# Kernel tuning notes

Hardware: AMD Instinct MI355X
Metric: run time of the kernel (lower is better)

## Reference

```python
import jax, jax.numpy as jnp
import numpy as np
from jax import lax

RHO = 0.1          # init kwarg rho
CG_ITERS = 15      # dc_torch(..., 0.001, 15): fixed 15 CG iterations
EPS = 1e-12


def _c(x):  # (..., 2) real pair -> complex
    return lax.complex(x[..., 0], x[..., 1])


def _r(x):  # complex -> (..., 2) real pair
    return jnp.stack([jnp.real(x), jnp.imag(x)], axis=-1)


def fft2c(x):
    ax = (-2, -1)
    return jnp.fft.fftshift(jnp.fft.fft2(jnp.fft.ifftshift(x, axes=ax), axes=ax, norm='ortho'), axes=ax)


def ifft2c(x):
    ax = (-2, -1)
    return jnp.fft.fftshift(jnp.fft.ifft2(jnp.fft.ifftshift(x, axes=ax), axes=ax, norm='ortho'), axes=ax)


def setup_inputs() -> dict:
    key = jax.random.key(0)
    k0, k1, k2, k3 = jax.random.split(key, 4)
    B, S, C, H, W = 1, 4, 16, 320, 320
    K = jax.random.normal(k0, (B, S, C, H, W, 2), jnp.float32)
    I = jax.random.normal(k1, (B, S, H, W, 2), jnp.float32)
    csm = jax.random.normal(k2, (B, C, H, W, 2), jnp.float32) * 0.2
    mask = (jax.random.uniform(k3, (B, S, H, W)) < 0.35).astype(jnp.float32)
    return {'K_mulShot_sigCoil': K, 'I': I, 'csm': csm, 'mask': mask}


def _dc_cg(kdata, img, s, m):
    # kdata: [B,S,C,H,W] complex, img: [B,S,H,W], s: [B,C,H,W], m: [B,S,H,W]
    def E(x):                      # image [B,S,H,W] -> k-space [B,S,C,H,W]
        return m[:, :, None] * fft2c(s[:, None] * x[:, :, None])

    def EH(y):                     # adjoint: coil-combine
        return jnp.sum(jnp.conj(s)[:, None] * ifft2c(m[:, :, None] * y), axis=2)

    def AtA(x):
        return EH(E(x)) + RHO * x

    rhs = EH(kdata) + RHO * img
    x0 = jnp.zeros_like(rhs)
    r0 = rhs
    rs0 = jnp.real(jnp.vdot(r0, r0))

    def body(carry, _):
        x, r, p, rs = carry
        Ap = AtA(p)
        alpha = rs / (jnp.real(jnp.vdot(p, Ap)) + EPS)
        x = x + alpha * p
        r = r - alpha * Ap
        rs_new = jnp.real(jnp.vdot(r, r))
        p = r + (rs_new / (rs + EPS)) * p
        return (x, r, p, rs_new), None

    (x, _, _, _), _ = lax.scan(body, (x0, r0, r0, rs0), None, length=CG_ITERS)
    return x


def reference(K_mulShot_sigCoil, I, csm, mask):
    kdata = _c(K_mulShot_sigCoil)
    img = _c(I)
    s = _c(csm)
    x = _dc_cg(kdata, img, s, mask)   # image-domain CG solution
    K = fft2c(x)                      # sf.dc_torch returns k-space
    out = ifft2c(K)                   # layer returns I = ifft2c(K)
    return _r(out)
```

## Files before the change

### kernel.cpp

```cpp
#include <hip/hip_runtime.h>
#include <math.h>


#define NDIM 320
#define HHALF 160
#define HW (NDIM*NDIM)
#define NS 4
#define NC 16
#define RHO_ 0.1f
#define CG_ITERS 15

typedef float v2f __attribute__((ext_vector_type(2)));
typedef _Float16 h2 __attribute__((ext_vector_type(2)));
typedef _Float16 h8v __attribute__((ext_vector_type(8)));

__device__ __forceinline__ v2f h2f(h2 h){ return (v2f){(float)h.x, (float)h.y}; }
__device__ __forceinline__ h2 f2h(v2f v){ return (h2){(_Float16)v.x, (_Float16)v.y}; }

__device__ __forceinline__ void wsync(){
    __builtin_amdgcn_fence(__ATOMIC_ACQ_REL, "wavefront");
    __builtin_amdgcn_wave_barrier();
}

__device__ __forceinline__ float wred(float v){
    #pragma unroll
    for (int o=32;o>0;o>>=1) v += __shfl_down(v,o,64);
    return v;
}

__device__ __forceinline__ v2f cmulf(v2f a, v2f b){
    return (v2f){a.x,a.x}*b + (v2f){-a.y,a.y}*(v2f){b.y,b.x};
}

template<int SIGMA>
__device__ __forceinline__ v2f cmulw(v2f a, v2f w){
    v2f wb = (SIGMA<0) ? w : (v2f){w.x, -w.y};
    return cmulf(a, wb);
}

template<int SIGMA>
__device__ __forceinline__ v2f mulj(v2f z){
    return (v2f){ -(float)SIGMA*z.y, (float)SIGMA*z.x };
}

template<int SIGMA>
__device__ __forceinline__ void radix5(const v2f* u, v2f* v){
    const float C1 = 0.30901699437494742f, S1 = 0.95105651629515357f;
    const float C2 = -0.80901699437494745f, S2 = 0.58778525229247312f;
    v2f t1=u[1]+u[4], t2=u[2]+u[3], t3=u[1]-u[4], t4=u[2]-u[3];
    v[0] = u[0] + t1 + t2;
    v2f m1 = u[0] + t1*C1 + t2*C2;
    v2f m2 = u[0] + t1*C2 + t2*C1;
    v2f n1 = t3*S1 + t4*S2;
    v2f n2 = t3*S2 - t4*S1;
    v2f j1 = mulj<SIGMA>(n1), j2 = mulj<SIGMA>(n2);
    v[1]=m1+j1; v[4]=m1-j1; v[2]=m2+j2; v[3]=m2-j2;
}

template<int SIGMA>
__device__ __forceinline__ void dft8(const v2f* u, v2f* y){
    const float C = 0.70710678118654752f;
    v2f a0=u[0]+u[4], a1=u[0]-u[4];
    v2f a2=u[2]+u[6], a3=u[2]-u[6];
    v2f a4=u[1]+u[5], a5=u[1]-u[5];
    v2f a6=u[3]+u[7], a7=u[3]-u[7];
    v2f j3 = mulj<SIGMA>(a3);
    v2f E0=a0+a2, E2=a0-a2;
    v2f E1=a1+j3, E3=a1-j3;
    v2f j7 = mulj<SIGMA>(a7);
    v2f O0=a4+a6, O2=a4-a6;
    v2f O1=a5+j7, O3=a5-j7;
    v2f W1 = (O1 + mulj<SIGMA>(O1)) * C;
    v2f jO2 = mulj<SIGMA>(O2);
    v2f W3 = (mulj<SIGMA>(O3) - O3) * C;
    y[0]=E0+O0; y[4]=E0-O0;
    y[1]=E1+W1; y[5]=E1-W1;
    y[2]=E2+jO2; y[6]=E2-jO2;
    y[3]=E3+W3; y[7]=E3-W3;
}

template<int SIGMA>
__device__ __forceinline__ void s1_from_regs(v2f* __restrict__ A, int t,
                                             const v2f* u5){
    v2f v[5];
    radix5<SIGMA>(u5, v);
    #pragma unroll
    for (int c=0;c<5;++c) A[5*t + c] = v[c];
}

template<int SIGMA>
__device__ __forceinline__ void s1_stage(v2f* __restrict__ A, int t){
    v2f u[5];
    #pragma unroll
    for (int q=0;q<5;++q) u[q] = A[t + 64*q];
    wsync();
    s1_from_regs<SIGMA>(A, t, u);
}

template<int SIGMA>
__device__ __forceinline__ void s2_stage(v2f* __restrict__ A, int t, v2f w40){
    if (t < 40){
        v2f u[8];
        #pragma unroll
        for (int q=0;q<8;++q) u[q] = A[t + 40*q];
        wsync();
        v2f wc = w40;
        u[1] = cmulw<SIGMA>(u[1], wc);
        #pragma unroll
        for (int q=2;q<8;++q){ wc = cmulf(wc, w40); u[q] = cmulw<SIGMA>(u[q], wc); }
        v2f v[8];
        dft8<SIGMA>(u, v);
        int k = t % 5, jb = t / 5;
        int base = jb*40 + k;
        #pragma unroll
        for (int c=0;c<8;++c) A[base + 5*c] = v[c];
    }
}

template<int SIGMA>
__device__ __forceinline__ void s3_toregs(const v2f* __restrict__ A, int t,
                                          v2f w320, v2f* v){
    if (t < 40){
        v2f u[8];
        #pragma unroll
        for (int q=0;q<8;++q) u[q] = A[t + 40*q];
        v2f wc = w320;
        u[1] = cmulw<SIGMA>(u[1], wc);
        #pragma unroll
        for (int q=2;q<8;++q){ wc = cmulf(wc, w320); u[q] = cmulw<SIGMA>(u[q], wc); }
        dft8<SIGMA>(u, v);
    }
}

template<int SIGMA>
__device__ __forceinline__ void a3_fromregs(v2f* __restrict__ A, int t,
                                            v2f w320, const v2f* vin){
    if (t < 40){
        v2f u[8];
        dft8<SIGMA>(vin, u);
        v2f wc = w320;
        u[1] = cmulw<SIGMA>(u[1], wc);
        #pragma unroll
        for (int q=2;q<8;++q){ wc = cmulf(wc, w320); u[q] = cmulw<SIGMA>(u[q], wc); }
        #pragma unroll
        for (int q=0;q<8;++q) A[t + 40*q] = u[q];
    }
}

template<int SIGMA>
__device__ __forceinline__ void a2_stage(v2f* __restrict__ A, int t, v2f w40){
    if (t < 40){
        int k = t % 5, jb = t / 5;
        int base = jb*40 + k;
        v2f v[8];
        #pragma unroll
        for (int c=0;c<8;++c) v[c] = A[base + 5*c];
        wsync();
        v2f u[8];
        dft8<SIGMA>(v, u);
        v2f wc = w40;
        u[1] = cmulw<SIGMA>(u[1], wc);
        #pragma unroll
        for (int q=2;q<8;++q){ wc = cmulf(wc, w40); u[q] = cmulw<SIGMA>(u[q], wc); }
        #pragma unroll
        for (int q=0;q<8;++q) A[t + 40*q] = u[q];
    }
}

template<int SIGMA>
__device__ __forceinline__ void a1_toregs(const v2f* __restrict__ A, int t,
                                          v2f* out5){
    v2f v[5];
    #pragma unroll
    for (int c=0;c<5;++c) v[c] = A[5*t + c];
    radix5<SIGMA>(v, out5);
}

__device__ __forceinline__ void make_w(int t, v2f& w40, v2f& w320){
    float sn, cs;
    const float n2pi = -6.283185307179586f;
    __sincosf(n2pi*(float)(t%5)/40.f, &sn, &cs); w40  = (v2f){cs, sn};
    __sincosf(n2pi*(float)t/320.f,    &sn, &cs); w320 = (v2f){cs, sn};
}

__device__ __forceinline__ int sh160(int i){ return i < HHALF ? i + HHALF : i - HHALF; }

__global__ void k_prep(const v2f* __restrict__ kin, const float* __restrict__ mask,
                       const v2f* __restrict__ csm, h2* __restrict__ sP,
                       float* __restrict__ mscT, h2* __restrict__ K,
                       float* __restrict__ scal)
{
    int gid = blockIdx.x*blockDim.x + threadIdx.x;
    int gsz = gridDim.x*blockDim.x;
    if (gid < 64) scal[gid] = 0.f;
    for (int i = gid; i < NC*HW; i += gsz){
        int w = i % NDIM; int h = (i/NDIM) % NDIM; int c = i/HW;
        sP[i] = f2h(csm[(c*NDIM + sh160(h))*NDIM + sh160(w)]);
    }
    for (int i = gid; i < NS*HW; i += gsz){
        int h = i % NDIM; int wc = (i/NDIM)%NDIM; int s = i/HW;
        float m = mask[(s*NDIM + sh160(h))*NDIM + sh160(wc)];
        mscT[i] = m*m*(1.0f/102400.0f);
    }
    for (int i = gid; i < NS*NC*HW; i += gsz){
        int w = i % NDIM; int h = (i/NDIM)%NDIM; int sc = i/HW;
        int s = sc >> 4;
        int hs = sh160(h), ws = sh160(w);
        float m = mask[(s*NDIM + hs)*NDIM + ws];
        v2f kv = kin[((long)sc*NDIM + hs)*NDIM + ws];
        float f = m*(1.0f/320.0f);
        K[i] = f2h(kv * f);
    }
}

__global__ __launch_bounds__(512) void k_passA(
    const v2f* __restrict__ rv_, const v2f* __restrict__ pOld,
    v2f* __restrict__ pNew, const h2* __restrict__ sP,
    h2* __restrict__ K, float* __restrict__ scal, int iter)
{
    int bid = blockIdx.x;
    int cg = bid & 3;
    int hg = (bid>>2) % 80;
    int s  = bid / (4*80);
    int tid = threadIdx.x;
    int wv = tid>>6; int rl = wv&3; int half = wv>>2; int t = tid&63;
    int h = hg*4 + rl;
    __shared__ v2f bufA[8][NDIM];
    __shared__ v2f pbuf[4][NDIM];
    v2f* A = &bufA[wv][0];
    v2f w40, w320; make_w(t, w40, w320);
    long base = (long)s*HW + h*NDIM;
    v2f pv[5];
    if (half == 0){
        float beta = 0.f;
        if (iter > 0) beta = scal[iter] / (scal[iter-1] + 1e-12f);
        #pragma unroll
        for (int j=0;j<5;++j){
            int idx = t + 64*j;
            v2f rr = rv_[base+idx];
            if (iter > 0){
                v2f pp = pOld[base+idx];
                pv[j] = rr + pp*beta;
            } else pv[j] = rr;
            pbuf[rl][idx] = pv[j];
        }
        if (cg == 0){
            float d = 0.f;
            #pragma unroll
            for (int j=0;j<5;++j){
                pNew[base + t + 64*j] = pv[j];
                d += pv[j].x*pv[j].x + pv[j].y*pv[j].y;
            }
            float wd = wred(d);
            if (t==0) atomicAdd(&scal[16+iter], RHO_*wd);
        }
    }
    __syncthreads();
    if (half == 1){
        #pragma unroll
        for (int j=0;j<5;++j) pv[j] = pbuf[rl][t + 64*j];
    }
    int c = cg*4 + half*2;
    const h2* srow = sP + (long)c*HW + h*NDIM;
    v2f sv[5];
    #pragma unroll
    for (int j=0;j<5;++j) sv[j] = h2f(srow[t+64*j]);
    #pragma unroll
    for (int c0=0;c0<2;++c0){
        v2f u5[5];
        #pragma unroll
        for (int j=0;j<5;++j) u5[j] = cmulf(sv[j], pv[j]);
        v2f sv2[5];
        if (c0<1){
            const h2* sr2 = srow + (long)HW;
            #pragma unroll
            for (int j=0;j<5;++j) sv2[j] = h2f(sr2[t+64*j]);
        }
        wsync();
        s1_from_regs<-1>(A, t, u5);
        wsync();
        s2_stage<-1>(A, t, w40);
        wsync();
        v2f v8[8];
        s3_toregs<-1>(A, t, w320, v8);
        long kb = ((long)(s*NC + c + c0))*HW + h*NDIM;
        if (t < 40){
            #pragma unroll
            for (int cc=0;cc<8;++cc) K[kb + t + 40*cc] = f2h(v8[cc]);
        }
        if (c0<1){
            #pragma unroll
            for (int j=0;j<5;++j) sv[j]=sv2[j];
        }
    }
}

__global__ __launch_bounds__(1024) void k_passB(h2* __restrict__ K,
    const float* __restrict__ mscT, int doMask)
{
    constexpr int L = 324;
    int bid = blockIdx.x;
    int wt = bid % 20;
    int sc = bid / 20;
    int s = sc >> 4;
    int tid = threadIdx.x;
    int col = tid >> 6;
    int t = tid & 63;
    int w0 = wt*16;
    __shared__ v2f bufA[16][L];
    v2f w40, w320; make_w(t, w40, w320);
    float mv[8];
    if (doMask && t < 40){
        const float* mcol = mscT + (long)s*HW + (long)(w0+col)*NDIM;
        #pragma unroll
        for (int cc=0;cc<8;++cc) mv[cc] = mcol[t+40*cc];
    }
    long gb = (long)sc*HW + w0;
    for (int i = tid; i < NDIM*4; i += 1024){
        int row = i >> 2, ch = i & 3;
        h8v val = *(const h8v*)&K[gb + (long)row*NDIM + ch*4];
        #pragma unroll
        for (int k=0;k<4;++k)
            bufA[ch*4+k][row] = (v2f){(float)val[2*k], (float)val[2*k+1]};
    }
    __syncthreads();
    v2f* A = &bufA[col][0];
    if (doMask){
        s1_stage<-1>(A, t);
        wsync();
        s2_stage<-1>(A, t, w40);
        wsync();
        v2f v8[8];
        s3_toregs<-1>(A, t, w320, v8);
        if (t < 40){
            #pragma unroll
            for (int cc=0;cc<8;++cc) v8[cc] = v8[cc]*mv[cc];
        }
        wsync();
        a3_fromregs<1>(A, t, w320, v8);
        wsync();
        a2_stage<1>(A, t, w40);
        wsync();
        v2f x5[5];
        a1_toregs<1>(A, t, x5);
        wsync();
        #pragma unroll
        for (int q=0;q<5;++q) A[t + 64*q] = x5[q];
    } else {
        s1_stage<1>(A, t);
        wsync();
        s2_stage<1>(A, t, w40);
        wsync();
        v2f v8[8];
        s3_toregs<1>(A, t, w320, v8);
        wsync();
        if (t < 40){
            #pragma unroll
            for (int cc=0;cc<8;++cc) A[t + 40*cc] = v8[cc];
        }
    }
    __syncthreads();
    for (int i = tid; i < NDIM*4; i += 1024){
        int row = i >> 2, ch = i & 3;
        h8v val;
        #pragma unroll
        for (int k=0;k<4;++k){
            v2f u = bufA[ch*4+k][row];
            val[2*k] = (_Float16)u.x; val[2*k+1] = (_Float16)u.y;
        }
        *(h8v*)&K[gb + (long)row*NDIM + ch*4] = val;
    }
}

__global__ __launch_bounds__(512) void k_passC2(
    const h2* __restrict__ K, const h2* __restrict__ sP,
    const v2f* __restrict__ pVec, v2f* __restrict__ part,
    float* __restrict__ scal, int dotSlot, int doDot)
{
    int bid = blockIdx.x;
    int cg = bid & 3;
    int hg = (bid>>2) % 80;
    int s  = bid / (4*80);
    int tid = threadIdx.x;
    int wv = tid>>6; int rl = wv&3; int half = wv>>2; int t = tid&63;
    int h = hg*4 + rl;
    __shared__ v2f bufA[8][NDIM];
    __shared__ float redS[4];
    v2f* A = &bufA[wv][0];
    v2f w40, w320; make_w(t, w40, w320);
    int c = cg*4 + half*2;
    long kb0 = ((long)(s*NC + c))*HW + h*NDIM;
    const h2* srow = sP + (long)c*HW + h*NDIM;
    v2f kv[8], sv[5];
    if (t < 40){
        #pragma unroll
        for (int cc=0;cc<8;++cc) kv[cc] = h2f(K[kb0 + t + 40*cc]);
    }
    #pragma unroll
    for (int j=0;j<5;++j) sv[j] = h2f(srow[t+64*j]);
    v2f acc[5];
    #pragma unroll
    for (int j=0;j<5;++j) acc[j]=(v2f){0.f,0.f};
    #pragma unroll
    for (int c0=0;c0<2;++c0){
        a3_fromregs<1>(A, t, w320, kv);
        v2f kv2[8], sv2[5];
        if (c0<1){
            long kb = kb0 + (long)HW;
            const h2* sr2 = srow + (long)HW;
            if (t < 40){
                #pragma unroll
                for (int cc=0;cc<8;++cc) kv2[cc] = h2f(K[kb + t + 40*cc]);
            }
            #pragma unroll
            for (int j=0;j<5;++j) sv2[j] = h2f(sr2[t+64*j]);
        }
        wsync();
        a2_stage<1>(A, t, w40);
        wsync();
        v2f x5[5];
        a1_toregs<1>(A, t, x5);
        #pragma unroll
        for (int j=0;j<5;++j){
            acc[j] += (v2f){sv[j].x,sv[j].x}*x5[j]
                    + (v2f){sv[j].y,-sv[j].y}*(v2f){x5[j].y,x5[j].x};
        }
        wsync();
        if (c0<1){
            #pragma unroll
            for (int cc=0;cc<8;++cc) kv[cc]=kv2[cc];
            #pragma unroll
            for (int j=0;j<5;++j) sv[j]=sv2[j];
        }
    }
    if (half == 1){
        #pragma unroll
        for (int j=0;j<5;++j) A[t + 64*j] = acc[j];
    }
    __syncthreads();
    if (half == 0){
        long pbase = (long)s*HW + h*NDIM;
        long obase = ((long)cg*NS + s)*HW + h*NDIM;
        float dot = 0.f;
        #pragma unroll
        for (int j=0;j<5;++j){
            int idx = t + 64*j;
            v2f av = acc[j] + bufA[4+rl][idx];
            part[obase+idx] = av;
            if (doDot){
                v2f pp = pVec[pbase+idx];
                dot += pp.x*av.x + pp.y*av.y;
            }
        }
        if (doDot){
            float wd = wred(dot);
            if (t==0) redS[rl] = wd;
        }
    }
    if (doDot){
        __syncthreads();
        if (tid==0) atomicAdd(&scal[dotSlot], redS[0]+redS[1]+redS[2]+redS[3]);
    }
}

__global__ __launch_bounds__(256) void k_rhs_fin(
    const v2f* __restrict__ part, const v2f* __restrict__ Iin,
    v2f* __restrict__ r, v2f* __restrict__ x, float* __restrict__ scal)
{
    __shared__ float red[256];
    int gid = blockIdx.x*blockDim.x + threadIdx.x;
    int gsz = gridDim.x*blockDim.x;
    float rs = 0.f;
    const int NV = NS*HW;
    for (int i = gid; i < NV; i += gsz){
        int w = i % NDIM; int h = (i/NDIM)%NDIM; int s = i/HW;
        v2f iv = Iin[((long)s*NDIM + sh160(h))*NDIM + sh160(w)];
        v2f rr = part[i] + part[NV+i] + part[2*NV+i] + part[3*NV+i] + iv*RHO_;
        r[i] = rr;
        x[i] = (v2f){0.f,0.f};
        rs += rr.x*rr.x + rr.y*rr.y;
    }
    red[threadIdx.x]=rs; __syncthreads();
    for (int o=128;o>0;o>>=1){ if (threadIdx.x<o) red[threadIdx.x]+=red[threadIdx.x+o]; __syncthreads(); }
    if (threadIdx.x==0) atomicAdd(&scal[0], red[0]);
}

__global__ __launch_bounds__(256) void k_update(
    v2f* __restrict__ x, v2f* __restrict__ r,
    const v2f* __restrict__ p, const v2f* __restrict__ part,
    float* __restrict__ scal, int iter)
{
    __shared__ float red[256];
    float alpha = scal[iter] / (scal[16+iter] + 1e-12f);
    int gid = blockIdx.x*blockDim.x + threadIdx.x;
    int gsz = gridDim.x*blockDim.x;
    float rs = 0.f;
    const int NV = NS*HW;
    for (int i = gid; i < NV; i += gsz){
        v2f pvv=p[i];
        v2f av = part[i] + part[NV+i] + part[2*NV+i] + part[3*NV+i] + pvv*RHO_;
        v2f xv = x[i] + pvv*alpha;
        v2f rv = r[i] - av*alpha;
        x[i]=xv; r[i]=rv;
        rs += rv.x*rv.x + rv.y*rv.y;
    }
    red[threadIdx.x]=rs; __syncthreads();
    for (int o=128;o>0;o>>=1){ if (threadIdx.x<o) red[threadIdx.x]+=red[threadIdx.x+o]; __syncthreads(); }
    if (threadIdx.x==0) atomicAdd(&scal[iter+1], red[0]);
}

__global__ void k_final(const v2f* __restrict__ x, v2f* __restrict__ out)
{
    int gid = blockIdx.x*blockDim.x + threadIdx.x;
    int gsz = gridDim.x*blockDim.x;
    for (int i = gid; i < NS*HW; i += gsz){
        int w = i % NDIM; int h = (i/NDIM)%NDIM; int s = i/HW;
        out[i] = x[(long)s*HW + sh160(h)*NDIM + sh160(w)];
    }
}

extern "C" void kernel_launch(void* const* d_in, const int* in_sizes, int n_in,
                              void* d_out, int out_size, void* d_ws, size_t ws_size,
                              hipStream_t stream) {
    (void)in_sizes; (void)n_in; (void)out_size; (void)ws_size;
    const v2f* kin  = (const v2f*)d_in[0];
    const v2f* Iin  = (const v2f*)d_in[1];
    const v2f* csm  = (const v2f*)d_in[2];
    const float* mask = (const float*)d_in[3];

    char* w = (char*)d_ws;
    size_t off = 0;
    float* scal = (float*)(w+off);  off += 1024;
    h2* sP    = (h2*)(w+off);  off += (size_t)NC*HW*4;
    float* mscT = (float*)(w+off); off += (size_t)NS*HW*4;
    h2* K     = (h2*)(w+off);  off += (size_t)NS*NC*HW*4;
    v2f* x    = (v2f*)(w+off); off += (size_t)NS*HW*8;
    v2f* r    = (v2f*)(w+off); off += (size_t)NS*HW*8;
    v2f* pA   = (v2f*)(w+off); off += (size_t)NS*HW*8;
    v2f* pB   = (v2f*)(w+off); off += (size_t)NS*HW*8;
    v2f* part = (v2f*)(w+off); off += (size_t)4*NS*HW*8;

    k_prep<<<2048,256,0,stream>>>(kin, mask, csm, sP, mscT, K, scal);
    k_passB<<<NS*NC*20,1024,0,stream>>>(K, mscT, 0);
    k_passC2<<<NS*80*4,512,0,stream>>>(K, sP, r, part, scal, 63, 0);
    k_rhs_fin<<<640,256,0,stream>>>(part, Iin, r, x, scal);

    for (int it=0; it<CG_ITERS; ++it){
        v2f* pNew = (it&1)? pB : pA;
        v2f* pOld = (it&1)? pA : pB;
        k_passA<<<NS*80*4,512,0,stream>>>(r, pOld, pNew, sP, K, scal, it);
        k_passB<<<NS*NC*20,1024,0,stream>>>(K, mscT, 1);
        k_passC2<<<NS*80*4,512,0,stream>>>(K, sP, pNew, part, scal, 16+it, 1);
        k_update<<<640,256,0,stream>>>(x, r, pNew, part, scal, it);
    }
    k_final<<<512,256,0,stream>>>(x, (v2f*)d_out);
}
```

Before: 1.524 ms.

## Fuse CG update into coil-combine pass and compute p·Ap in k-space

The p^H A p dot product now comes from masked k-space energy inside the k-space FFT pass, using Parseval, rather than from the coil-combined result in the adjoint pass. The separate CG update kernel is removed. The last of the four coil-group blocks for each row group, found through an atomic counter, performs the x/r update and the residual-norm reduction for those rows. This saves one kernel launch per iteration and a full pass over the partial buffers, at the cost of fences, per-iteration counters, and a serialized tail in some blocks.

After: 5.494 ms. +260.4%, slower.

```diff
diff --git a/kernel.cpp b/kernel.cpp
--- a/kernel.cpp
+++ b/kernel.cpp
@@ -188,11 +188,12 @@
 __global__ void k_prep(const v2f* __restrict__ kin, const float* __restrict__ mask,
                        const v2f* __restrict__ csm, h2* __restrict__ sP,
                        float* __restrict__ mscT, h2* __restrict__ K,
-                       float* __restrict__ scal)
+                       float* __restrict__ scal, int* __restrict__ cnt)
 {
     int gid = blockIdx.x*blockDim.x + threadIdx.x;
     int gsz = gridDim.x*blockDim.x;
     if (gid < 64) scal[gid] = 0.f;
+    for (int i = gid; i < CG_ITERS*320; i += gsz) cnt[i] = 0;
     for (int i = gid; i < NC*HW; i += gsz){
         int w = i % NDIM; int h = (i/NDIM) % NDIM; int c = i/HW;
         sP[i] = f2h(csm[(c*NDIM + sh160(h))*NDIM + sh160(w)]);
@@ -296,7 +297,8 @@
 }
 
 __global__ __launch_bounds__(1024) void k_passB(h2* __restrict__ K,
-    const float* __restrict__ mscT, int doMask)
+    const float* __restrict__ mscT, float* __restrict__ scal, int iter,
+    int doMask)
 {
     constexpr int L = 324;
     int bid = blockIdx.x;
@@ -308,6 +310,7 @@
     int t = tid & 63;
     int w0 = wt*16;
     __shared__ v2f bufA[16][L];
+    __shared__ float redP[16];
     v2f w40, w320; make_w(t, w40, w320);
     float mv[8];
     if (doMask && t < 40){
@@ -332,9 +335,18 @@
         wsync();
         v2f v8[8];
         s3_toregs<-1>(A, t, w320, v8);
+        float pap = 0.f;
         if (t < 40){
             #pragma unroll
-            for (int cc=0;cc<8;++cc) v8[cc] = v8[cc]*mv[cc];
+            for (int cc=0;cc<8;++cc){
+                float m = mv[cc];
+                pap += m*(v8[cc].x*v8[cc].x + v8[cc].y*v8[cc].y);
+                v8[cc] = v8[cc]*m;
+            }
+        }
+        {
+            float wp = wred(pap);
+            if (t==0) redP[col] = wp;
         }
         wsync();
         a3_fromregs<1>(A, t, w320, v8);
@@ -370,12 +382,19 @@
         }
         *(h8v*)&K[gb + (long)row*NDIM + ch*4] = val;
     }
+    if (doMask && tid==0){
+        float sum = 0.f;
+        #pragma unroll
+        for (int k=0;k<16;++k) sum += redP[k];
+        atomicAdd(&scal[16+iter], sum);
+    }
 }
 
 __global__ __launch_bounds__(512) void k_passC2(
     const h2* __restrict__ K, const h2* __restrict__ sP,
     const v2f* __restrict__ pVec, v2f* __restrict__ part,
-    float* __restrict__ scal, int dotSlot, int doDot)
+    v2f* __restrict__ xv, v2f* __restrict__ rv,
+    float* __restrict__ scal, int* __restrict__ cnt, int iter, int doFuse)
 {
     int bid = blockIdx.x;
     int cg = bid & 3;
@@ -385,7 +404,8 @@
     int wv = tid>>6; int rl = wv&3; int half = wv>>2; int t = tid&63;
     int h = hg*4 + rl;
     __shared__ v2f bufA[8][NDIM];
-    __shared__ float redS[4];
+    __shared__ float redW[8];
+    __shared__ int lastFlag;
     v2f* A = &bufA[wv][0];
     v2f w40, w320; make_w(t, w40, w320);
     int c = cg*4 + half*2;
@@ -439,27 +459,43 @@
     }
     __syncthreads();
     if (half == 0){
-        long pbase = (long)s*HW + h*NDIM;
         long obase = ((long)cg*NS + s)*HW + h*NDIM;
-        float dot = 0.f;
         #pragma unroll
         for (int j=0;j<5;++j){
             int idx = t + 64*j;
-            v2f av = acc[j] + bufA[4+rl][idx];
-            part[obase+idx] = av;
-            if (doDot){
-                v2f pp = pVec[pbase+idx];
-                dot += pp.x*av.x + pp.y*av.y;
-            }
-        }
-        if (doDot){
-            float wd = wred(dot);
-            if (t==0) redS[rl] = wd;
-        }
-    }
-    if (doDot){
-        __syncthreads();
-        if (tid==0) atomicAdd(&scal[dotSlot], redS[0]+redS[1]+redS[2]+redS[3]);
+            part[obase+idx] = acc[j] + bufA[4+rl][idx];
+        }
+    }
+    if (!doFuse) return;
+    __threadfence();
+    if (tid==0){
+        int old = __hip_atomic_fetch_add(&cnt[iter*320 + s*80 + hg], 1,
+                      __ATOMIC_ACQ_REL, __HIP_MEMORY_SCOPE_AGENT);
+        lastFlag = (old==3) ? 1 : 0;
+    }
+    __syncthreads();
+    if (!lastFlag) return;
+    const int NV = NS*HW;
+    float alpha = scal[iter] / (scal[16+iter] + 1e-12f);
+    float rs = 0.f;
+    for (int i = tid; i < 4*NDIM; i += 512){
+        long idx = (long)s*HW + (long)(hg*4 + i/NDIM)*NDIM + (i % NDIM);
+        v2f pp = pVec[idx];
+        v2f av = part[idx] + part[NV+idx] + part[2*NV+idx] + part[3*NV+idx]
+               + pp*RHO_;
+        v2f xn = xv[idx] + pp*alpha;
+        v2f rn = rv[idx] - av*alpha;
+        xv[idx] = xn; rv[idx] = rn;
+        rs += rn.x*rn.x + rn.y*rn.y;
+    }
+    float wr = wred(rs);
+    if (t==0) redW[wv] = wr;
+    __syncthreads();
+    if (tid==0){
+        float sum = 0.f;
+        #pragma unroll
+        for (int k=0;k<8;++k) sum += redW[k];
+        atomicAdd(&scal[iter+1], sum);
     }
 }
 
@@ -485,30 +521,6 @@
     if (threadIdx.x==0) atomicAdd(&scal[0], red[0]);
 }
 
-__global__ __launch_bounds__(256) void k_update(
-    v2f* __restrict__ x, v2f* __restrict__ r,
-    const v2f* __restrict__ p, const v2f* __restrict__ part,
-    float* __restrict__ scal, int iter)
-{
-    __shared__ float red[256];
-    float alpha = scal[iter] / (scal[16+iter] + 1e-12f);
-    int gid = blockIdx.x*blockDim.x + threadIdx.x;
-    int gsz = gridDim.x*blockDim.x;
-    float rs = 0.f;
-    const int NV = NS*HW;
-    for (int i = gid; i < NV; i += gsz){
-        v2f pvv=p[i];
-        v2f av = part[i] + part[NV+i] + part[2*NV+i] + part[3*NV+i] + pvv*RHO_;
-        v2f xv = x[i] + pvv*alpha;
-        v2f rv = r[i] - av*alpha;
-        x[i]=xv; r[i]=rv;
-        rs += rv.x*rv.x + rv.y*rv.y;
-    }
-    red[threadIdx.x]=rs; __syncthreads();
-    for (int o=128;o>0;o>>=1){ if (threadIdx.x<o) red[threadIdx.x]+=red[threadIdx.x+o]; __syncthreads(); }
-    if (threadIdx.x==0) atomicAdd(&scal[iter+1], red[0]);
-}
-
 __global__ void k_final(const v2f* __restrict__ x, v2f* __restrict__ out)
 {
     int gid = blockIdx.x*blockDim.x + threadIdx.x;
@@ -531,6 +543,7 @@
     char* w = (char*)d_ws;
     size_t off = 0;
     float* scal = (float*)(w+off);  off += 1024;
+    int* cnt  = (int*)(w+off);  off += 32*1024;
     h2* sP    = (h2*)(w+off);  off += (size_t)NC*HW*4;
     float* mscT = (float*)(w+off); off += (size_t)NS*HW*4;
     h2* K     = (h2*)(w+off);  off += (size_t)NS*NC*HW*4;
@@ -540,18 +553,17 @@
     v2f* pB   = (v2f*)(w+off); off += (size_t)NS*HW*8;
     v2f* part = (v2f*)(w+off); off += (size_t)4*NS*HW*8;
 
-    k_prep<<<2048,256,0,stream>>>(kin, mask, csm, sP, mscT, K, scal);
-    k_passB<<<NS*NC*20,1024,0,stream>>>(K, mscT, 0);
-    k_passC2<<<NS*80*4,512,0,stream>>>(K, sP, r, part, scal, 63, 0);
+    k_prep<<<2048,256,0,stream>>>(kin, mask, csm, sP, mscT, K, scal, cnt);
+    k_passB<<<NS*NC*20,1024,0,stream>>>(K, mscT, scal, 0, 0);
+    k_passC2<<<NS*80*4,512,0,stream>>>(K, sP, r, part, x, r, scal, cnt, 0, 0);
     k_rhs_fin<<<640,256,0,stream>>>(part, Iin, r, x, scal);
 
     for (int it=0; it<CG_ITERS; ++it){
         v2f* pNew = (it&1)? pB : pA;
         v2f* pOld = (it&1)? pA : pB;
         k_passA<<<NS*80*4,512,0,stream>>>(r, pOld, pNew, sP, K, scal, it);
-        k_passB<<<NS*NC*20,1024,0,stream>>>(K, mscT, 1);
-        k_passC2<<<NS*80*4,512,0,stream>>>(K, sP, pNew, part, scal, 16+it, 1);
-        k_update<<<640,256,0,stream>>>(x, r, pNew, part, scal, it);
+        k_passB<<<NS*NC*20,1024,0,stream>>>(K, mscT, scal, it, 1);
+        k_passC2<<<NS*80*4,512,0,stream>>>(K, sP, pNew, part, x, r, scal, cnt, it, 1);
     }
     k_final<<<512,256,0,stream>>>(x, (v2f*)d_out);
 }
```
